# Kernel optimization log

Measured on AMD Instinct MI355X. Metric: run time of the kernel, lower is better.

Reference implementation:

```python
import jax, jax.numpy as jnp
import numpy as np

SVL = 0.5        # spatial_volume_length
FVL = 0.86603    # frustum_volume_length
IMG = 256        # input_image_size
FD = 48          # frustum_volume_depth
FS = IMG // 8    # frustum_volume_size = 32


def grid_sample_3d(vol, grid):
    """Trilinear grid_sample, padding_mode='zeros', align_corners=True.
    vol: (B,C,Dv,Hv,Wv); grid: (B,D,H,W,3), last dim = (x,y,z) in [-1,1]
    where x indexes Wv, y indexes Hv, z indexes Dv. Returns (B,C,D,H,W)."""
    B, C, Dv, Hv, Wv = vol.shape
    sp = grid.shape[1:4]
    x = (grid[..., 0] + 1.0) * 0.5 * (Wv - 1)
    y = (grid[..., 1] + 1.0) * 0.5 * (Hv - 1)
    z = (grid[..., 2] + 1.0) * 0.5 * (Dv - 1)
    x0f, y0f, z0f = jnp.floor(x), jnp.floor(y), jnp.floor(z)
    xd, yd, zd = x - x0f, y - y0f, z - z0f
    x0, y0, z0 = x0f.astype(jnp.int32), y0f.astype(jnp.int32), z0f.astype(jnp.int32)
    vol_flat = vol.reshape(B, C, Dv * Hv * Wv)
    gather = jax.vmap(lambda vf, ix: vf[:, ix])  # (C,M),(K,) -> (C,K)
    out = jnp.zeros((B, C) + sp, vol.dtype)
    for dz in (0, 1):
        for dy in (0, 1):
            for dx in (0, 1):
                xi, yi, zi = x0 + dx, y0 + dy, z0 + dz
                valid = (xi >= 0) & (xi < Wv) & (yi >= 0) & (yi < Hv) & (zi >= 0) & (zi < Dv)
                w = ((xd if dx else 1.0 - xd)
                     * (yd if dy else 1.0 - yd)
                     * (zd if dz else 1.0 - zd))
                w = jnp.where(valid, w, 0.0)
                idx = ((jnp.clip(zi, 0, Dv - 1) * Hv + jnp.clip(yi, 0, Hv - 1)) * Wv
                       + jnp.clip(xi, 0, Wv - 1))
                g = gather(vol_flat, idx.reshape(B, -1)).reshape((B, C) + sp)
                out = out + w[:, None] * g
    return out


def setup_inputs() -> dict:
    key = jax.random.key(0)
    k1, k2, k3, k4 = jax.random.split(key, 4)
    B, N, TN, C, V = 2, 16, 8, 64, 32
    return {
        "spatial_volume": jax.random.normal(k1, (B, C, V, V, V), dtype=jnp.float32),
        "target_RT": jax.random.normal(k2, (B, N, 3, 4), dtype=jnp.float32),
        "target_K": jax.random.normal(k3, (B, N, 4, 4), dtype=jnp.float32),
        "target_indices": jax.random.randint(k4, (B, TN), 0, N),
    }


def reference(spatial_volume, target_RT, target_K, target_indices):
    B, C, V = spatial_volume.shape[0], spatial_volume.shape[1], spatial_volume.shape[2]
    TN = target_indices.shape[1]
    BT = B * TN
    H = W = FS
    D = FD
    dt = spatial_volume.dtype

    # camera centers: -R^T t, distances to origin
    R = target_RT[..., :3, :3]                  # B,N,3,3
    T = target_RT[..., :3, 3]                   # B,N,3
    cam_pos = -jnp.einsum('bnji,bnj->bni', R, T)
    cam_dist = jnp.linalg.norm(cam_pos, axis=-1)  # B,N

    # gather per-target-view pose / K / distance
    bidx = jnp.arange(B)[:, None]
    poses = target_RT[bidx, target_indices].reshape(BT, 3, 4)
    Ks = target_K[bidx, target_indices].reshape(BT, 4, 4)
    dist = cam_dist[bidx, target_indices].reshape(BT)
    near, far = dist - FVL, dist + FVL

    # per-ray depth values (constant across pixels since near/far are scalar per view)
    tlin = jnp.linspace(0.0, 1.0, D, dtype=dt)
    depth = near[:, None] + tlin[None, :] * (far - near)[:, None]   # BT,D

    # pixel grid at frustum resolution, scaled to input-image pixel coords
    ys, xs = jnp.meshgrid(jnp.arange(H, dtype=dt), jnp.arange(W, dtype=dt), indexing='ij')
    pix = jnp.stack([xs, ys, jnp.ones_like(xs)], 0).reshape(1, 3, H * W)
    scale = jnp.array([IMG / FS, IMG / FS, 1.0], dtype=dt).reshape(1, 3, 1)
    pix = pix * scale                                                # 1,3,HW
    pts = pix[:, :, None, :] * depth[:, None, :, None]               # BT,3,D,HW

    # unproject homogeneous image points through inverse(K @ [R|t])
    P = jnp.einsum('bij,bjk->bik', Ks[:, :3, :3], poses)             # BT,3,4
    bottom = jnp.broadcast_to(jnp.array([0.0, 0.0, 0.0, 1.0], dtype=dt).reshape(1, 1, 4), (BT, 1, 4))
    P4 = jnp.concatenate([P, bottom], axis=1)
    Pinv = jnp.linalg.inv(P4)
    xyz = jnp.einsum('bij,bjk->bik', Pinv[:, :3, :3], pts.reshape(BT, 3, D * H * W)) + Pinv[:, :3, 3:]

    # normalize world coords to [-1,1] of the spatial volume and sample
    grid = (xyz / SVL).reshape(BT, 3, D, H, W).transpose(0, 2, 3, 4, 1)  # BT,D,H,W,3
    sv = jnp.broadcast_to(spatial_volume[:, None], (B, TN, C, V, V, V)).reshape(BT, C, V, V, V)
    feats = grid_sample_3d(sv, grid)                                  # BT,C,D,H,W
    depth_vol = jnp.broadcast_to(depth[:, :, None, None], (BT, D, H, W))
    return feats, depth_vol
```

## Files before the change

kernel.cpp:

```cpp
#include <hip/hip_runtime.h>
#include <cstdint>

#define BB   2
#define NN   16
#define TNN  8
#define BT   16
#define CC   64
#define VV   32
#define V3   (VV*VV*VV)
#define DD   48
#define HH   32
#define WW   32
#define FVL_ 0.86603

__global__ void setup_params(const float* __restrict__ RT, const float* __restrict__ Km,
                             const int* __restrict__ tidx, float* __restrict__ params) {
    int bt = threadIdx.x;
    if (bt >= BT) return;
    int b = bt / TNN, j = bt % TNN;
    int n = tidx[b * TNN + j];
    const float* pose = RT + (size_t)(b * NN + n) * 12;
    const float* K    = Km + (size_t)(b * NN + n) * 16;

    double T0 = pose[3], T1 = pose[7], T2 = pose[11];
    double cp0 = -((double)pose[0] * T0 + (double)pose[4] * T1 + (double)pose[8]  * T2);
    double cp1 = -((double)pose[1] * T0 + (double)pose[5] * T1 + (double)pose[9]  * T2);
    double cp2 = -((double)pose[2] * T0 + (double)pose[6] * T1 + (double)pose[10] * T2);
    double dist = sqrt(cp0*cp0 + cp1*cp1 + cp2*cp2);
    double nearv = dist - FVL_;
    double step  = 2.0 * FVL_ / (DD - 1);

    double A[3][3], bv[3];
    #pragma unroll
    for (int i = 0; i < 3; ++i) {
        #pragma unroll
        for (int jj = 0; jj < 3; ++jj)
            A[i][jj] = (double)K[i*4+0]*pose[0*4+jj] + (double)K[i*4+1]*pose[1*4+jj]
                     + (double)K[i*4+2]*pose[2*4+jj];
        bv[i] = (double)K[i*4+0]*pose[3] + (double)K[i*4+1]*pose[7] + (double)K[i*4+2]*pose[11];
    }
    double c00 =  A[1][1]*A[2][2] - A[1][2]*A[2][1];
    double c01 =  A[1][2]*A[2][0] - A[1][0]*A[2][2];
    double c02 =  A[1][0]*A[2][1] - A[1][1]*A[2][0];
    double det = A[0][0]*c00 + A[0][1]*c01 + A[0][2]*c02;
    double Mi[3][3];
    Mi[0][0] = c00 / det;
    Mi[0][1] = (A[0][2]*A[2][1] - A[0][1]*A[2][2]) / det;
    Mi[0][2] = (A[0][1]*A[1][2] - A[0][2]*A[1][1]) / det;
    Mi[1][0] = c01 / det;
    Mi[1][1] = (A[0][0]*A[2][2] - A[0][2]*A[2][0]) / det;
    Mi[1][2] = (A[0][2]*A[1][0] - A[0][0]*A[1][2]) / det;
    Mi[2][0] = c02 / det;
    Mi[2][1] = (A[0][1]*A[2][0] - A[0][0]*A[2][1]) / det;
    Mi[2][2] = (A[0][0]*A[1][1] - A[0][1]*A[1][0]) / det;
    double tv[3];
    #pragma unroll
    for (int i = 0; i < 3; ++i)
        tv[i] = -(Mi[i][0]*bv[0] + Mi[i][1]*bv[1] + Mi[i][2]*bv[2]);

    const double s = 31.0;
    float* p = params + bt * 16;
    #pragma unroll
    for (int i = 0; i < 3; ++i) {
        p[i*4+0] = (float)(s * Mi[i][0] * 8.0);
        p[i*4+1] = (float)(s * Mi[i][1] * 8.0);
        p[i*4+2] = (float)(s * Mi[i][2]);
        p[i*4+3] = (float)(s * tv[i] + 15.5);
    }
    p[12] = (float)nearv;
    p[13] = (float)step;
}

__global__ __launch_bounds__(256) void transpose_vol2(const float* __restrict__ vol,
                                                      float* __restrict__ volT) {
    __shared__ float tl[64 * 65];
    int b    = blockIdx.x >> 9;
    int tile = blockIdx.x & 511;
    size_t zyx0 = (size_t)tile << 6;
    int l  = threadIdx.x & 63;
    int gq = threadIdx.x >> 6;
    #pragma unroll
    for (int k = 0; k < 16; ++k) {
        int c = (gq << 4) + k;
        tl[l * 65 + c] = vol[(((size_t)(b * 64 + c)) << 15) + zyx0 + l];
    }
    __syncthreads();
    #pragma unroll
    for (int k = 0; k < 16; ++k) {
        int zy = (gq << 4) + k;
        volT[((size_t)b << 21) + ((zyx0 + zy) << 6) + l] = tl[zy * 65 + l];
    }
}

__global__ __launch_bounds__(512) void sample_cl2(const float* __restrict__ volT,
                                                  const float* __restrict__ params,
                                                  float* __restrict__ feats,
                                                  float* __restrict__ depthv) {
    __shared__ float lds[32 * 68];
    int t   = threadIdx.x;
    int blk = blockIdx.x;
    int h  = blk & 31;
    int t2 = blk >> 5;
    int d  = t2 % DD;
    int bt = t2 / DD;
    int b  = bt >> 3;

    const float* p = params + bt * 16;
    float depth = fmaf(p[13], (float)d, p[12]);

    int lane = t & 63;
    int wv   = t >> 6;
    int pp   = lane >> 4;
    int q    = lane & 15;
    int w    = (wv << 2) | pp;

    float fw = (float)w, fh = (float)h;
    float cx = fmaf(depth, fmaf(p[0], fw, fmaf(p[1], fh, p[2])),  p[3]);
    float cy = fmaf(depth, fmaf(p[4], fw, fmaf(p[5], fh, p[6])),  p[7]);
    float cz = fmaf(depth, fmaf(p[8], fw, fmaf(p[9], fh, p[10])), p[11]);

    float acc0 = 0.f, acc1 = 0.f, acc2 = 0.f, acc3 = 0.f;
    bool inside = (cx > -1.f) && (cx < 32.f) && (cy > -1.f) && (cy < 32.f)
               && (cz > -1.f) && (cz < 32.f);
    if (inside) {
        float xf = floorf(cx), yf = floorf(cy), zf = floorf(cz);
        int x0 = (int)xf, y0 = (int)yf, z0 = (int)zf;
        float xd = cx - xf, yd = cy - yf, zd = cz - zf;
        int x0c = max(x0, 0), x1c = min(x0 + 1, 31);
        int y0c = max(y0, 0), y1c = min(y0 + 1, 31);
        int z0c = max(z0, 0), z1c = min(z0 + 1, 31);
        float wx0 = (x0     >= 0)  ? 1.f - xd : 0.f;
        float wx1 = (x0 + 1 <= 31) ? xd       : 0.f;
        float wy0 = (y0     >= 0)  ? 1.f - yd : 0.f;
        float wy1 = (y0 + 1 <= 31) ? yd       : 0.f;
        float wz0 = (z0     >= 0)  ? 1.f - zd : 0.f;
        float wz1 = (z0 + 1 <= 31) ? zd       : 0.f;

        const float* vb = volT + (((size_t)b << 21)) + (q << 2);
        #define CORNER(zc, yc, xc, WGT) do {                                        \
            const float4 v = *reinterpret_cast<const float4*>(                       \
                vb + ((((size_t)(zc) * 32 + (yc)) * 32 + (xc)) << 6));               \
            float wg = (WGT);                                                        \
            acc0 = fmaf(wg, v.x, acc0);  acc1 = fmaf(wg, v.y, acc1);                 \
            acc2 = fmaf(wg, v.z, acc2);  acc3 = fmaf(wg, v.w, acc3);                 \
        } while (0)
        CORNER(z0c, y0c, x0c, wz0 * wy0 * wx0);
        CORNER(z0c, y0c, x1c, wz0 * wy0 * wx1);
        CORNER(z0c, y1c, x0c, wz0 * wy1 * wx0);
        CORNER(z0c, y1c, x1c, wz0 * wy1 * wx1);
        CORNER(z1c, y0c, x0c, wz1 * wy0 * wx0);
        CORNER(z1c, y0c, x1c, wz1 * wy0 * wx1);
        CORNER(z1c, y1c, x0c, wz1 * wy1 * wx0);
        CORNER(z1c, y1c, x1c, wz1 * wy1 * wx1);
        #undef CORNER
    }

    float4 av = {acc0, acc1, acc2, acc3};
    *reinterpret_cast<float4*>(&lds[w * 68 + (q << 2)]) = av;
    __syncthreads();

    int w2 = t & 31;
    int g  = t >> 5;
    float4 rv = *reinterpret_cast<const float4*>(&lds[w2 * 68 + (g << 2)]);
    const size_t CHs = (size_t)DD * HH * WW;
    size_t o = (((size_t)(bt * CC + (g << 2)) * DD + d) * (HH * WW)) + h * WW + w2;
    feats[o]           = rv.x;
    feats[o + CHs]     = rv.y;
    feats[o + 2 * CHs] = rv.z;
    feats[o + 3 * CHs] = rv.w;
    if (t < 32)
        depthv[((size_t)bt * DD + d) * (HH * WW) + h * WW + t] = depth;
}

__global__ __launch_bounds__(512) void sample_fallback(const float* __restrict__ vol,
                                                       const float* __restrict__ params,
                                                       float* __restrict__ feats,
                                                       float* __restrict__ depthv) {
    int w  = threadIdx.x;
    int ty = threadIdx.y;
    int blk = blockIdx.x;
    int h  = blk & 31;
    int t2 = blk >> 5;
    int d  = t2 % DD;
    int bt = t2 / DD;
    int b  = bt >> 3;

    const float* p = params + bt * 16;
    float depth = fmaf(p[13], (float)d, p[12]);
    float fw = (float)w, fh = (float)h;
    float cx = fmaf(depth, fmaf(p[0], fw, fmaf(p[1], fh, p[2])),  p[3]);
    float cy = fmaf(depth, fmaf(p[4], fw, fmaf(p[5], fh, p[6])),  p[7]);
    float cz = fmaf(depth, fmaf(p[8], fw, fmaf(p[9], fh, p[10])), p[11]);

    float accs[4] = {0.f, 0.f, 0.f, 0.f};
    bool inside = (cx > -1.f) && (cx < 32.f) && (cy > -1.f) && (cy < 32.f)
               && (cz > -1.f) && (cz < 32.f);
    if (inside) {
        float xf = floorf(cx), yf = floorf(cy), zf = floorf(cz);
        int x0 = (int)xf, y0 = (int)yf, z0 = (int)zf;
        float xd = cx - xf, yd = cy - yf, zd = cz - zf;
        int x0c = max(x0, 0), x1c = min(x0 + 1, 31);
        int y0c = max(y0, 0), y1c = min(y0 + 1, 31);
        int z0c = max(z0, 0), z1c = min(z0 + 1, 31);
        float wx0 = (x0     >= 0)  ? 1.f - xd : 0.f;
        float wx1 = (x0 + 1 <= 31) ? xd       : 0.f;
        float wy0 = (y0     >= 0)  ? 1.f - yd : 0.f;
        float wy1 = (y0 + 1 <= 31) ? yd       : 0.f;
        float wz0 = (z0     >= 0)  ? 1.f - zd : 0.f;
        float wz1 = (z0 + 1 <= 31) ? zd       : 0.f;
        int o000 = ((z0c * 32) + y0c) * 32 + x0c;
        int o001 = ((z0c * 32) + y0c) * 32 + x1c;
        int o010 = ((z0c * 32) + y1c) * 32 + x0c;
        int o011 = ((z0c * 32) + y1c) * 32 + x1c;
        int o100 = ((z1c * 32) + y0c) * 32 + x0c;
        int o101 = ((z1c * 32) + y0c) * 32 + x1c;
        int o110 = ((z1c * 32) + y1c) * 32 + x0c;
        int o111 = ((z1c * 32) + y1c) * 32 + x1c;
        float w000 = wz0*wy0*wx0, w001 = wz0*wy0*wx1, w010 = wz0*wy1*wx0, w011 = wz0*wy1*wx1;
        float w100 = wz1*wy0*wx0, w101 = wz1*wy0*wx1, w110 = wz1*wy1*wx0, w111 = wz1*wy1*wx1;
        #pragma unroll
        for (int k = 0; k < 4; ++k) {
            const float* vc = vol + (size_t)(b * CC + (ty << 2) + k) * V3;
            float a = 0.f;
            a = fmaf(w000, vc[o000], a); a = fmaf(w001, vc[o001], a);
            a = fmaf(w010, vc[o010], a); a = fmaf(w011, vc[o011], a);
            a = fmaf(w100, vc[o100], a); a = fmaf(w101, vc[o101], a);
            a = fmaf(w110, vc[o110], a); a = fmaf(w111, vc[o111], a);
            accs[k] = a;
        }
    }
    const size_t CHs = (size_t)DD * HH * WW;
    size_t o = (((size_t)bt * CC + (ty << 2)) * DD + d) * (HH * WW) + h * WW + w;
    feats[o]           = accs[0];
    feats[o + CHs]     = accs[1];
    feats[o + 2 * CHs] = accs[2];
    feats[o + 3 * CHs] = accs[3];
    if (ty == 0)
        depthv[((size_t)bt * DD + d) * (HH * WW) + h * WW + w] = depth;
}

extern "C" void kernel_launch(void* const* d_in, const int* in_sizes, int n_in,
                              void* d_out, int out_size, void* d_ws, size_t ws_size,
                              hipStream_t stream) {
    const float* vol  = (const float*)d_in[0];
    const float* RT   = (const float*)d_in[1];
    const float* Km   = (const float*)d_in[2];
    const int*   tidx = (const int*)d_in[3];

    float* feats  = (float*)d_out;
    float* depthv = feats + (size_t)BT * CC * DD * HH * WW;

    float* params = (float*)d_ws;
    float* volT   = (float*)((char*)d_ws + 4096);
    const size_t volT_bytes = (size_t)BB * CC * V3 * sizeof(float);
    bool use_cl = ws_size >= 4096 + volT_bytes;

    setup_params<<<1, 64, 0, stream>>>(RT, Km, tidx, params);
    if (use_cl) {
        transpose_vol2<<<BB * (V3 / 64), 256, 0, stream>>>(vol, volT);
        sample_cl2<<<BT * DD * HH, 512, 0, stream>>>(volT, params, feats, depthv);
    } else {
        sample_fallback<<<BT * DD * HH, dim3(32, 16, 1), 0, stream>>>(vol, params, feats, depthv);
    }
}
```

Baseline: 220.8 us.

## Store transposed volume as bf16 and sample two rows per block

The channel-last volume copy is now rounded to bf16 during the transpose, which halves the bytes fetched per trilinear corner gather. Each sampling thread now loads 8 channels as one 16-byte load, and each block covers two image rows (64 pixels), so there are half as many blocks. Output writes still go through LDS and are coalesced over 64 pixels. This adds bf16 rounding error to the features, which may exceed the reference tolerance. The main output write of about 200MB fp32 is unchanged, so the gain is limited to gather traffic.

```diff
diff --git a/kernel.cpp b/kernel.cpp
--- a/kernel.cpp
+++ b/kernel.cpp
@@ -71,9 +71,9 @@
     p[13] = (float)step;
 }
 
-__global__ __launch_bounds__(256) void transpose_vol2(const float* __restrict__ vol,
-                                                      float* __restrict__ volT) {
-    __shared__ float tl[64 * 65];
+__global__ __launch_bounds__(256) void convert_transpose(const float* __restrict__ vol,
+                                                         ushort* __restrict__ volTb) {
+    __shared__ ushort tl[64 * 66];
     int b    = blockIdx.x >> 9;
     int tile = blockIdx.x & 511;
     size_t zyx0 = (size_t)tile << 6;
@@ -82,25 +82,27 @@
     #pragma unroll
     for (int k = 0; k < 16; ++k) {
         int c = (gq << 4) + k;
-        tl[l * 65 + c] = vol[(((size_t)(b * 64 + c)) << 15) + zyx0 + l];
+        float v = vol[(((size_t)(b * 64 + c)) << 15) + zyx0 + l];
+        uint32_t u = __float_as_uint(v);
+        tl[l * 66 + c] = (ushort)((u + 0x7fffu + ((u >> 16) & 1u)) >> 16);
     }
     __syncthreads();
     #pragma unroll
     for (int k = 0; k < 16; ++k) {
         int zy = (gq << 4) + k;
-        volT[((size_t)b << 21) + ((zyx0 + zy) << 6) + l] = tl[zy * 65 + l];
-    }
-}
-
-__global__ __launch_bounds__(512) void sample_cl2(const float* __restrict__ volT,
-                                                  const float* __restrict__ params,
-                                                  float* __restrict__ feats,
-                                                  float* __restrict__ depthv) {
-    __shared__ float lds[32 * 68];
+        volTb[((size_t)b << 21) + ((zyx0 + zy) << 6) + l] = tl[zy * 66 + l];
+    }
+}
+
+__global__ __launch_bounds__(512) void sample_bf16(const ushort* __restrict__ volTb,
+                                                   const float* __restrict__ params,
+                                                   float* __restrict__ feats,
+                                                   float* __restrict__ depthv) {
+    __shared__ float lds[64 * 65];
     int t   = threadIdx.x;
     int blk = blockIdx.x;
-    int h  = blk & 31;
-    int t2 = blk >> 5;
+    int hp = blk & 15;
+    int t2 = blk >> 4;
     int d  = t2 % DD;
     int bt = t2 / DD;
     int b  = bt >> 3;
@@ -110,16 +112,18 @@
 
     int lane = t & 63;
     int wv   = t >> 6;
-    int pp   = lane >> 4;
-    int q    = lane & 15;
-    int w    = (wv << 2) | pp;
+    int pp   = lane >> 3;
+    int q    = lane & 7;
+    int pidx = (wv << 3) | pp;
+    int w    = pidx & 31;
+    int h    = (hp << 1) | (pidx >> 5);
 
     float fw = (float)w, fh = (float)h;
     float cx = fmaf(depth, fmaf(p[0], fw, fmaf(p[1], fh, p[2])),  p[3]);
     float cy = fmaf(depth, fmaf(p[4], fw, fmaf(p[5], fh, p[6])),  p[7]);
     float cz = fmaf(depth, fmaf(p[8], fw, fmaf(p[9], fh, p[10])), p[11]);
 
-    float acc0 = 0.f, acc1 = 0.f, acc2 = 0.f, acc3 = 0.f;
+    float acc[8] = {0.f, 0.f, 0.f, 0.f, 0.f, 0.f, 0.f, 0.f};
     bool inside = (cx > -1.f) && (cx < 32.f) && (cy > -1.f) && (cy < 32.f)
                && (cz > -1.f) && (cz < 32.f);
     if (inside) {
@@ -136,13 +140,19 @@
         float wz0 = (z0     >= 0)  ? 1.f - zd : 0.f;
         float wz1 = (z0 + 1 <= 31) ? zd       : 0.f;
 
-        const float* vb = volT + (((size_t)b << 21)) + (q << 2);
-        #define CORNER(zc, yc, xc, WGT) do {                                        \
-            const float4 v = *reinterpret_cast<const float4*>(                       \
-                vb + ((((size_t)(zc) * 32 + (yc)) * 32 + (xc)) << 6));               \
-            float wg = (WGT);                                                        \
-            acc0 = fmaf(wg, v.x, acc0);  acc1 = fmaf(wg, v.y, acc1);                 \
-            acc2 = fmaf(wg, v.z, acc2);  acc3 = fmaf(wg, v.w, acc3);                 \
+        const ushort* vb = volTb + ((size_t)b << 21) + (q << 3);
+        #define CORNER(zc, yc, xc, WGT) do {                                         \
+            const uint4 v = *reinterpret_cast<const uint4*>(                          \
+                vb + ((((size_t)(zc) * 32 + (yc)) * 32 + (xc)) << 6));                \
+            float wg = (WGT);                                                         \
+            acc[0] = fmaf(wg, __uint_as_float(v.x << 16),          acc[0]);           \
+            acc[1] = fmaf(wg, __uint_as_float(v.x & 0xffff0000u),  acc[1]);           \
+            acc[2] = fmaf(wg, __uint_as_float(v.y << 16),          acc[2]);           \
+            acc[3] = fmaf(wg, __uint_as_float(v.y & 0xffff0000u),  acc[3]);           \
+            acc[4] = fmaf(wg, __uint_as_float(v.z << 16),          acc[4]);           \
+            acc[5] = fmaf(wg, __uint_as_float(v.z & 0xffff0000u),  acc[5]);           \
+            acc[6] = fmaf(wg, __uint_as_float(v.w << 16),          acc[6]);           \
+            acc[7] = fmaf(wg, __uint_as_float(v.w & 0xffff0000u),  acc[7]);           \
         } while (0)
         CORNER(z0c, y0c, x0c, wz0 * wy0 * wx0);
         CORNER(z0c, y0c, x1c, wz0 * wy0 * wx1);
@@ -155,21 +165,22 @@
         #undef CORNER
     }
 
-    float4 av = {acc0, acc1, acc2, acc3};
-    *reinterpret_cast<float4*>(&lds[w * 68 + (q << 2)]) = av;
+    #pragma unroll
+    for (int j = 0; j < 8; ++j)
+        lds[pidx * 65 + (q << 3) + j] = acc[j];
     __syncthreads();
 
-    int w2 = t & 31;
-    int g  = t >> 5;
-    float4 rv = *reinterpret_cast<const float4*>(&lds[w2 * 68 + (g << 2)]);
-    const size_t CHs = (size_t)DD * HH * WW;
-    size_t o = (((size_t)(bt * CC + (g << 2)) * DD + d) * (HH * WW)) + h * WW + w2;
-    feats[o]           = rv.x;
-    feats[o + CHs]     = rv.y;
-    feats[o + 2 * CHs] = rv.z;
-    feats[o + 3 * CHs] = rv.w;
-    if (t < 32)
-        depthv[((size_t)bt * DD + d) * (HH * WW) + h * WW + t] = depth;
+    int pt = t & 63;
+    int c8 = t >> 6;
+    int h0 = hp << 1;
+    #pragma unroll
+    for (int j = 0; j < 8; ++j) {
+        int c = (c8 << 3) + j;
+        size_t o = (((size_t)(bt * CC + c) * DD + d) << 10) + (h0 << 5) + pt;
+        feats[o] = lds[pt * 65 + c];
+    }
+    if (t < 64)
+        depthv[(((size_t)bt * DD + d) << 10) + (h0 << 5) + t] = depth;
 }
 
 __global__ __launch_bounds__(512) void sample_fallback(const float* __restrict__ vol,
@@ -250,15 +261,15 @@
     float* feats  = (float*)d_out;
     float* depthv = feats + (size_t)BT * CC * DD * HH * WW;
 
-    float* params = (float*)d_ws;
-    float* volT   = (float*)((char*)d_ws + 4096);
-    const size_t volT_bytes = (size_t)BB * CC * V3 * sizeof(float);
-    bool use_cl = ws_size >= 4096 + volT_bytes;
+    float*  params = (float*)d_ws;
+    ushort* volTb  = (ushort*)((char*)d_ws + 4096);
+    const size_t volTb_bytes = (size_t)BB * CC * V3 * sizeof(ushort);
+    bool use_cl = ws_size >= 4096 + volTb_bytes;
 
     setup_params<<<1, 64, 0, stream>>>(RT, Km, tidx, params);
     if (use_cl) {
-        transpose_vol2<<<BB * (V3 / 64), 256, 0, stream>>>(vol, volT);
-        sample_cl2<<<BT * DD * HH, 512, 0, stream>>>(volT, params, feats, depthv);
+        convert_transpose<<<BB * (V3 / 64), 256, 0, stream>>>(vol, volTb);
+        sample_bf16<<<BT * DD * (HH / 2), 512, 0, stream>>>(volTb, params, feats, depthv);
     } else {
         sample_fallback<<<BT * DD * HH, dim3(32, 16, 1), 0, stream>>>(vol, params, feats, depthv);
     }
```

Result: no change. 218.5 us (-1.1%).
